# Performance work log

Hardware: AMD Instinct MI355X
Metric: run time of the kernel (lower is better)

## Reference

```python
import jax, jax.numpy as jnp
import numpy as np

T, B, D, H = 2048, 2, 1024, 16
NH, DH = H // 2, D // H   # 8 heads per direction, d_head = 64
DFF = 4096


def layer_norm(x, g, b, eps=1e-5):
    mu = jnp.mean(x, axis=-1, keepdims=True)
    var = jnp.mean(jnp.square(x - mu), axis=-1, keepdims=True)
    return (x - mu) * jax.lax.rsqrt(var + eps) * g + b


def rel_shift(x):
    # x: [q, k, b, n] -> Transformer-XL relative shift
    q, k, b, n = x.shape
    x = jnp.concatenate([jnp.zeros((q, 1, b, n), x.dtype), x], axis=1)
    return x.reshape(k + 1, q, b, n)[1:].reshape(q, k, b, n)


def rel_attn(w, r, mask, qkv_w, r_w, r_w_bias, r_r_bias):
    # w: [T, B, D], r: [R, 1, D], mask: [T, T] bool (True = masked)
    t, b, _ = w.shape
    heads = jnp.einsum('tbd,ed->tbe', w, qkv_w)              # [T,B,3*NH*DH]
    q, k, v = jnp.split(heads, 3, axis=-1)
    q = q.reshape(t, b, NH, DH)
    k = k.reshape(t, b, NH, DH)
    v = v.reshape(t, b, NH, DH)
    rk = jnp.einsum('rd,ed->re', r[:, 0, :], r_w).reshape(-1, NH, DH)  # [R,NH,DH]
    AC = jnp.einsum('ibnd,jbnd->ijbn', q + r_w_bias, k)
    BD = rel_shift(jnp.einsum('ibnd,jnd->ijbn', q + r_r_bias, rk))
    score = (AC + BD) * (1.0 / np.sqrt(DH))
    score = jnp.where(mask[:, :, None, None], jnp.finfo(score.dtype).min, score)
    prob = jax.nn.softmax(score, axis=1)
    vec = jnp.einsum('ijbn,jbnd->ibnd', prob, v)
    return vec.reshape(t, b, NH * DH)


def setup_inputs() -> dict:
    key = jax.random.key(0)
    ks = jax.random.split(key, 24)
    s = 0.02
    causal = jnp.triu(jnp.ones((T, T), dtype=bool), k=1)
    return {
        'x': jax.random.normal(ks[0], (T, B, D), jnp.float32),
        'pos': jax.random.normal(ks[1], (T, 1, D), jnp.float32),
        'mask_fwd': causal,
        'mask_bwd': causal,
        'ln1_g': jnp.ones((D,), jnp.float32), 'ln1_b': jnp.zeros((D,), jnp.float32),
        'ln2_g': jnp.ones((D,), jnp.float32), 'ln2_b': jnp.zeros((D,), jnp.float32),
        'ln3_g': jnp.ones((D,), jnp.float32), 'ln3_b': jnp.zeros((D,), jnp.float32),
        'qkv_f': jax.random.normal(ks[2], (3 * NH * DH, D), jnp.float32) * s,
        'rnet_f': jax.random.normal(ks[3], (NH * DH, D), jnp.float32) * s,
        'rwb_f': jax.random.normal(ks[4], (NH, DH), jnp.float32) * s,
        'rrb_f': jax.random.normal(ks[5], (NH, DH), jnp.float32) * s,
        'qkv_b': jax.random.normal(ks[6], (3 * NH * DH, D), jnp.float32) * s,
        'rnet_b': jax.random.normal(ks[7], (NH * DH, D), jnp.float32) * s,
        'rwb_b': jax.random.normal(ks[8], (NH, DH), jnp.float32) * s,
        'rrb_b': jax.random.normal(ks[9], (NH, DH), jnp.float32) * s,
        'wo': jax.random.normal(ks[10], (D, D), jnp.float32) * s,
        'bo': jnp.zeros((D,), jnp.float32),
        'w1': jax.random.normal(ks[11], (DFF, D), jnp.float32) * s,
        'b1': jnp.zeros((DFF,), jnp.float32),
        'w2': jax.random.normal(ks[12], (D, DFF), jnp.float32) * s,
        'b2': jnp.zeros((D,), jnp.float32),
    }


def reference(x, pos, mask_fwd, mask_bwd,
              ln1_g, ln1_b, ln2_g, ln2_b, ln3_g, ln3_b,
              qkv_f, rnet_f, rwb_f, rrb_f,
              qkv_b, rnet_b, rwb_b, rrb_b,
              wo, bo, w1, b1, w2, b2):
    # --- bidirectional relative attention ---
    q_fwd = layer_norm(x, ln1_g, ln1_b)
    q_bwd = layer_norm(jnp.flip(x, axis=0), ln2_g, ln2_b)
    out_fwd = rel_attn(q_fwd, pos, mask_fwd, qkv_f, rnet_f, rwb_f, rrb_f)
    out_bwd = rel_attn(q_bwd, pos, mask_bwd, qkv_b, rnet_b, rwb_b, rrb_b)
    out = jnp.concatenate([out_fwd, jnp.flip(out_bwd, axis=0)], axis=-1)
    out = jnp.einsum('tbd,ed->tbe', out, wo) + bo
    h = x + out                     # postprocess_attn: dropout(id) + residual
    # --- feed forward: LN -> Linear -> ReLU -> Linear -> residual ---
    y = layer_norm(h, ln3_g, ln3_b)
    y = jax.nn.relu(jnp.einsum('tbd,fd->tbf', y, w1) + b1)
    y = jnp.einsum('tbf,df->tbd', y, w2) + b2
    return h + y
```

## Files before the change

kernel.cpp:

```cpp
#include <hip/hip_runtime.h>
#include <cstdint>
#include <cstddef>


typedef unsigned short ushort_t;
typedef __bf16 bf16x8 __attribute__((ext_vector_type(8)));
typedef float f32x4 __attribute__((ext_vector_type(4)));
typedef float f32x16 __attribute__((ext_vector_type(16)));
typedef unsigned short us8 __attribute__((ext_vector_type(8)));
typedef unsigned short us4 __attribute__((ext_vector_type(4)));

#define DEV static __device__ __forceinline__

DEV ushort_t f2bf(float x) {
  union { float f; unsigned u; } v; v.f = x;
  unsigned r = (v.u + 0x7FFFu + ((v.u >> 16) & 1u)) >> 16;
  return (ushort_t)r;
}
DEV ushort_t f2bt(float x) {
  union { float f; unsigned u; } v; v.f = x;
  return (ushort_t)(v.u >> 16);
}
DEV float bf2f(ushort_t h) {
  union { unsigned u; float f; } v; v.u = ((unsigned)h) << 16;
  return v.f;
}
DEV float fexp2(float x) { float r; asm("v_exp_f32 %0, %1" : "=v"(r) : "v"(x)); return r; }
DEV f32x4 mfma16(bf16x8 a, bf16x8 b, f32x4 c) {
  return __builtin_amdgcn_mfma_f32_16x16x32_bf16(a, b, c, 0, 0, 0);
}
DEV f32x16 mfma32(bf16x8 a, bf16x8 b, f32x16 c) {
  return __builtin_amdgcn_mfma_f32_32x32x16_bf16(a, b, c, 0, 0, 0);
}
DEV void gld16(const void* g, void* l) {
  __builtin_amdgcn_global_load_lds((const __attribute__((address_space(1))) void*)g,
                                   (__attribute__((address_space(3))) void*)l,
                                   16, 0, 0);
}

constexpr size_t O_QKV_F  = 0;
constexpr size_t O_QKV_B  = 3145728;
constexpr size_t O_RNET_F = 6291456;
constexpr size_t O_RNET_B = 7340032;
constexpr size_t O_WO     = 8388608;
constexpr size_t O_W1     = 10485760;
constexpr size_t O_W2     = 18874368;
constexpr size_t O_RKREV_F= 27262976;
constexpr size_t O_RKREV_B= 29360128;
constexpr size_t O_QAC_F  = 31457280;
constexpr size_t O_QBD_F  = 35651584;
constexpr size_t O_KK_F   = 39845888;
constexpr size_t O_VT_F   = 44040192;
constexpr size_t O_QAC_B  = 48234496;
constexpr size_t O_QBD_B  = 52428800;
constexpr size_t O_KK_B   = 56623104;
constexpr size_t O_VT_B   = 60817408;
constexpr size_t O_H      = 65011712;
constexpr size_t O_LN3    = 81788928;
constexpr size_t ZONE     = 90177536;
constexpr size_t O_POS    = ZONE + 0;
constexpr size_t O_LN1    = ZONE + 4194304;
constexpr size_t O_LN2    = ZONE + 12582912;
constexpr size_t O_HEADS_F= ZONE + 20971520;
constexpr size_t O_HEADS_B= ZONE + 33554432;
constexpr size_t O_ACAT   = ZONE + 0;
constexpr size_t O_FFNM   = ZONE + 8388608;

struct CvtArgs {
  const float* src[8];
  ushort_t* dst[8];
  int bstart[8];
};
__global__ __launch_bounds__(256)
void cvt_all_k(CvtArgs a) {
  int bx = blockIdx.x;
  int s = 0;
#pragma unroll
  for (int k = 1; k < 8; ++k) if (bx >= a.bstart[k]) s = k;
  int i = (bx - a.bstart[s]) * 256 + threadIdx.x;
  float4 v = reinterpret_cast<const float4*>(a.src[s])[i];
  us4 o; o[0] = f2bf(v.x); o[1] = f2bf(v.y); o[2] = f2bf(v.z); o[3] = f2bf(v.w);
  reinterpret_cast<us4*>(a.dst[s])[i] = o;
}

__global__ __launch_bounds__(256)
void ln_dual_k(const float* __restrict__ x,
               const float* __restrict__ g1, const float* __restrict__ b1,
               const float* __restrict__ g2, const float* __restrict__ b2,
               ushort_t* __restrict__ o1, ushort_t* __restrict__ o2) {
  __shared__ float sbuf[8];
  const int row = blockIdx.x;
  const int tid = threadIdx.x;
  const float* xr = x + (size_t)row * 1024;
  float4 v = reinterpret_cast<const float4*>(xr)[tid];
  float s  = v.x + v.y + v.z + v.w;
  float s2 = v.x*v.x + v.y*v.y + v.z*v.z + v.w*v.w;
  for (int m = 32; m >= 1; m >>= 1) { s += __shfl_xor(s, m, 64); s2 += __shfl_xor(s2, m, 64); }
  int w = tid >> 6;
  if ((tid & 63) == 0) { sbuf[w] = s; sbuf[4 + w] = s2; }
  __syncthreads();
  float S  = sbuf[0] + sbuf[1] + sbuf[2] + sbuf[3];
  float S2 = sbuf[4] + sbuf[5] + sbuf[6] + sbuf[7];
  float mu  = S * (1.f / 1024.f);
  float var = S2 * (1.f / 1024.f) - mu * mu;
  float inv = rsqrtf(var + 1e-5f);
  int t = row >> 1, b = row & 1;
  size_t r2 = ((size_t)(2047 - t) * 2 + b) * 1024;
  float4 G1 = reinterpret_cast<const float4*>(g1)[tid];
  float4 B1 = reinterpret_cast<const float4*>(b1)[tid];
  float4 G2 = reinterpret_cast<const float4*>(g2)[tid];
  float4 B2 = reinterpret_cast<const float4*>(b2)[tid];
  float n0 = (v.x - mu) * inv, n1 = (v.y - mu) * inv, n2 = (v.z - mu) * inv, n3 = (v.w - mu) * inv;
  us4 a, c;
  a[0] = f2bf(n0 * G1.x + B1.x); a[1] = f2bf(n1 * G1.y + B1.y);
  a[2] = f2bf(n2 * G1.z + B1.z); a[3] = f2bf(n3 * G1.w + B1.w);
  c[0] = f2bf(n0 * G2.x + B2.x); c[1] = f2bf(n1 * G2.y + B2.y);
  c[2] = f2bf(n2 * G2.z + B2.z); c[3] = f2bf(n3 * G2.w + B2.w);
  reinterpret_cast<us4*>(o1 + (size_t)row * 1024)[tid] = a;
  reinterpret_cast<us4*>(o2 + r2)[tid] = c;
}

__global__ __launch_bounds__(256)
void ln_one_k(const float* __restrict__ x,
              const float* __restrict__ g1, const float* __restrict__ b1,
              ushort_t* __restrict__ o1) {
  __shared__ float sbuf[8];
  const int row = blockIdx.x;
  const int tid = threadIdx.x;
  const float* xr = x + (size_t)row * 1024;
  float4 v = reinterpret_cast<const float4*>(xr)[tid];
  float s  = v.x + v.y + v.z + v.w;
  float s2 = v.x*v.x + v.y*v.y + v.z*v.z + v.w*v.w;
  for (int m = 32; m >= 1; m >>= 1) { s += __shfl_xor(s, m, 64); s2 += __shfl_xor(s2, m, 64); }
  int w = tid >> 6;
  if ((tid & 63) == 0) { sbuf[w] = s; sbuf[4 + w] = s2; }
  __syncthreads();
  float S  = sbuf[0] + sbuf[1] + sbuf[2] + sbuf[3];
  float S2 = sbuf[4] + sbuf[5] + sbuf[6] + sbuf[7];
  float mu  = S * (1.f / 1024.f);
  float var = S2 * (1.f / 1024.f) - mu * mu;
  float inv = rsqrtf(var + 1e-5f);
  float4 G1 = reinterpret_cast<const float4*>(g1)[tid];
  float4 B1 = reinterpret_cast<const float4*>(b1)[tid];
  us4 a;
  a[0] = f2bf((v.x - mu) * inv * G1.x + B1.x);
  a[1] = f2bf((v.y - mu) * inv * G1.y + B1.y);
  a[2] = f2bf((v.z - mu) * inv * G1.z + B1.z);
  a[3] = f2bf((v.w - mu) * inv * G1.w + B1.w);
  reinterpret_cast<us4*>(o1 + (size_t)row * 1024)[tid] = a;
}

template <int EPI>
__global__ __launch_bounds__(256)
void gemm_bt(const ushort_t* __restrict__ A, const ushort_t* __restrict__ B,
             void* __restrict__ C, const float* __restrict__ bias,
             const float* __restrict__ resid, int M, int N, int K) {
  __shared__ ushort_t As[128 * 64];
  __shared__ ushort_t Bs[128 * 64];
  const int tid = threadIdx.x;
  const int lane = tid & 63;
  const int w = tid >> 6;
  const int wm = w >> 1, wn = w & 1;
  const int row0 = blockIdx.y * 128, col0 = blockIdx.x * 128;
  const int lr = lane & 15;
  const int lkb = (lane >> 4) * 8;
  const int rr = lane >> 3;
  const int scb = ((lane & 7) ^ rr) * 8;
  const f32x4 fz = {0.f, 0.f, 0.f, 0.f};
  f32x4 acc[4][4];
#pragma unroll
  for (int i = 0; i < 4; ++i)
#pragma unroll
    for (int j = 0; j < 4; ++j) acc[i][j] = fz;

  for (int k0 = 0; k0 < K; k0 += 64) {
    __syncthreads();
#pragma unroll
    for (int it = 0; it < 4; ++it) {
      int rbase = it * 32 + w * 8;
      gld16(A + (size_t)(row0 + rbase + rr) * K + k0 + scb, (char*)As + rbase * 128);
      gld16(B + (size_t)(col0 + rbase + rr) * K + k0 + scb, (char*)Bs + rbase * 128);
    }
    __syncthreads();
#pragma unroll
    for (int kk = 0; kk < 64; kk += 32) {
      bf16x8 af[4], bfr[4];
#pragma unroll
      for (int mi = 0; mi < 4; ++mi) {
        int r = wm * 64 + mi * 16 + lr;
        int off = (r * 128 + (kk + lkb) * 2) ^ ((r & 7) << 4);
        af[mi] = *reinterpret_cast<const bf16x8*>((char*)As + off);
      }
#pragma unroll
      for (int ni = 0; ni < 4; ++ni) {
        int r = wn * 64 + ni * 16 + lr;
        int off = (r * 128 + (kk + lkb) * 2) ^ ((r & 7) << 4);
        bfr[ni] = *reinterpret_cast<const bf16x8*>((char*)Bs + off);
      }
#pragma unroll
      for (int mi = 0; mi < 4; ++mi)
#pragma unroll
        for (int ni = 0; ni < 4; ++ni)
          acc[mi][ni] = mfma16(af[mi], bfr[ni], acc[mi][ni]);
    }
  }
#pragma unroll
  for (int mi = 0; mi < 4; ++mi)
#pragma unroll
    for (int ni = 0; ni < 4; ++ni)
#pragma unroll
      for (int r = 0; r < 4; ++r) {
        int row = row0 + wm * 64 + mi * 16 + (lane >> 4) * 4 + r;
        int col = col0 + wn * 64 + ni * 16 + lr;
        float v = acc[mi][ni][r];
        if (EPI == 0) {
          ((ushort_t*)C)[(size_t)row * N + col] = f2bf(v);
        } else if (EPI == 1) {
          v += bias[col]; v = v > 0.f ? v : 0.f;
          ((ushort_t*)C)[(size_t)row * N + col] = f2bf(v);
        } else {
          v += bias[col] + resid[(size_t)row * N + col];
          ((float*)C)[(size_t)row * N + col] = v;
        }
      }
}

template <int EPI>
__global__ __launch_bounds__(256)
void gemm64(const ushort_t* __restrict__ A0, const ushort_t* __restrict__ A1,
            const ushort_t* __restrict__ B0, const ushort_t* __restrict__ B1,
            void* __restrict__ C0, void* __restrict__ C1,
            const float* __restrict__ bias, const float* __restrict__ resid,
            int M, int N, int K) {
  __shared__ ushort_t As[64 * 64];
  __shared__ ushort_t Bs[128 * 64];
  const ushort_t* A = blockIdx.z ? A1 : A0;
  const ushort_t* B = blockIdx.z ? B1 : B0;
  void* C = blockIdx.z ? (void*)C1 : (void*)C0;
  const int tid = threadIdx.x;
  const int lane = tid & 63;
  const int w = tid >> 6;
  const int wm = w >> 1, wn = w & 1;
  const int row0 = blockIdx.y * 64, col0 = blockIdx.x * 128;
  const int lr = lane & 15;
  const int lkb = (lane >> 4) * 8;
  const int rr = lane >> 3;
  const int scb = ((lane & 7) ^ rr) * 8;
  const f32x4 fz = {0.f, 0.f, 0.f, 0.f};
  f32x4 acc[2][4];
#pragma unroll
  for (int i = 0; i < 2; ++i)
#pragma unroll
    for (int j = 0; j < 4; ++j) acc[i][j] = fz;

  for (int k0 = 0; k0 < K; k0 += 64) {
    __syncthreads();
#pragma unroll
    for (int it = 0; it < 2; ++it) {
      int rbase = it * 32 + w * 8;
      gld16(A + (size_t)(row0 + rbase + rr) * K + k0 + scb, (char*)As + rbase * 128);
    }
#pragma unroll
    for (int it = 0; it < 4; ++it) {
      int rbase = it * 32 + w * 8;
      gld16(B + (size_t)(col0 + rbase + rr) * K + k0 + scb, (char*)Bs + rbase * 128);
    }
    __syncthreads();
#pragma unroll
    for (int kk = 0; kk < 64; kk += 32) {
      bf16x8 af[2], bfr[4];
#pragma unroll
      for (int mi = 0; mi < 2; ++mi) {
        int r = wm * 32 + mi * 16 + lr;
        int off = (r * 128 + (kk + lkb) * 2) ^ ((r & 7) << 4);
        af[mi] = *reinterpret_cast<const bf16x8*>((char*)As + off);
      }
#pragma unroll
      for (int ni = 0; ni < 4; ++ni) {
        int r = wn * 64 + ni * 16 + lr;
        int off = (r * 128 + (kk + lkb) * 2) ^ ((r & 7) << 4);
        bfr[ni] = *reinterpret_cast<const bf16x8*>((char*)Bs + off);
      }
#pragma unroll
      for (int mi = 0; mi < 2; ++mi)
#pragma unroll
        for (int ni = 0; ni < 4; ++ni)
          acc[mi][ni] = mfma16(af[mi], bfr[ni], acc[mi][ni]);
    }
  }
#pragma unroll
  for (int mi = 0; mi < 2; ++mi)
#pragma unroll
    for (int ni = 0; ni < 4; ++ni)
#pragma unroll
      for (int r = 0; r < 4; ++r) {
        int row = row0 + wm * 32 + mi * 16 + (lane >> 4) * 4 + r;
        int col = col0 + wn * 64 + ni * 16 + lr;
        float v = acc[mi][ni][r];
        if (EPI == 0) {
          ((ushort_t*)C)[(size_t)row * N + col] = f2bf(v);
        } else if (EPI == 1) {
          v += bias[col]; v = v > 0.f ? v : 0.f;
          ((ushort_t*)C)[(size_t)row * N + col] = f2bf(v);
        } else if (EPI == 2) {
          v += bias[col] + resid[(size_t)row * N + col];
          ((float*)C)[(size_t)row * N + col] = v;
        } else {
          int nn = col >> 6, dh = col & 63;
          ((ushort_t*)C)[((size_t)nn * 2048 + (2047 - row)) * 64 + dh] = f2bf(v);
        }
      }
}

__global__ __launch_bounds__(256)
void qkv_post2_k(const ushort_t* __restrict__ hf, const ushort_t* __restrict__ hb2,
                 const float* __restrict__ rwf, const float* __restrict__ rrf,
                 const float* __restrict__ rwb2, const float* __restrict__ rrb2,
                 char* __restrict__ wsb) {
  const float SCL = 0.125f * 1.44269504088896f;
  const int dir = blockIdx.y;
  const ushort_t* heads = dir ? hb2 : hf;
  const float* rwb = dir ? rwb2 : rwf;
  const float* rrb = dir ? rrb2 : rrf;
  ushort_t* q_ac = (ushort_t*)(wsb + (dir ? O_QAC_B : O_QAC_F));
  ushort_t* q_bd = (ushort_t*)(wsb + (dir ? O_QBD_B : O_QBD_F));
  ushort_t* kout = (ushort_t*)(wsb + (dir ? O_KK_B : O_KK_F));
  int row = blockIdx.x;
  int t = row >> 1, b = row & 1;
#pragma unroll
  for (int c0 = 0; c0 < 1024; c0 += 256) {
    int c = c0 + threadIdx.x;
    ushort_t hv = heads[(size_t)row * 1536 + c];
    if (c < 512) {
      int n = c >> 6, dh = c & 63;
      size_t o = ((size_t)(b * 8 + n) * 2048 + t) * 64 + dh;
      float q = bf2f(hv);
      q_ac[o] = f2bf((q + rwb[c]) * SCL);
      q_bd[o] = f2bf((q + rrb[c]) * SCL);
    } else {
      int cc = c - 512;
      int n = cc >> 6, dh = cc & 63;
      kout[((size_t)(b * 8 + n) * 2048 + t) * 64 + dh] = hv;
    }
  }
}

__global__ __launch_bounds__(256)
void v_trans2_k(const ushort_t* __restrict__ hf, const ushort_t* __restrict__ hb2,
                char* __restrict__ wsb) {
  __shared__ float tile[64][65];
  const int dir = blockIdx.z;
  const ushort_t* heads = dir ? hb2 : hf;
  ushort_t* vt = (ushort_t*)(wsb + (dir ? O_VT_B : O_VT_F));
  int tt0 = blockIdx.x * 64;
  int bn = blockIdx.y;
  int b = bn >> 3, n = bn & 7;
  int tid = threadIdx.x;
#pragma unroll
  for (int i = 0; i < 16; ++i) {
    int rr = i * 4 + (tid >> 6);
    int cc = tid & 63;
    tile[rr][cc] = bf2f(heads[(size_t)((tt0 + rr) * 2 + b) * 1536 + 1024 + n * 64 + cc]);
  }
  __syncthreads();
#pragma unroll
  for (int i = 0; i < 16; ++i) {
    int dh = i * 4 + (tid >> 6);
    int tt = tid & 63;
    vt[((size_t)bn * 64 + dh) * 2048 + tt0 + tt] = f2bf(tile[tt][dh]);
  }
}

__global__ __launch_bounds__(256, 2)
void attn_k(const char* __restrict__ wsb, ushort_t* __restrict__ outp) {
  __shared__ ushort_t Kbuf[2][64 * 64];
  __shared__ ushort_t Vbuf[2][64 * 64];
  __shared__ ushort_t Gs[4][32 * 100];

  const int tid = threadIdx.x;
  const int lane = tid & 63;
  const int w = tid >> 6;
  const int il = lane & 31;
  const int hi = lane >> 5;
  const int rr = lane >> 3;
  const int scb = ((lane & 7) ^ rr) * 8;

  const int id = (int)(blockIdx.x + (blockIdx.y << 4) + (blockIdx.z << 8));
  const int xcd = id & 7;
  const int ord = id >> 3;
  const int pair = xcd * 4 + (ord & 3);
  const int it = 15 - (ord >> 2);
  const int bn = pair & 15;
  const int dir = pair >> 4;

  const ushort_t* qac  = (const ushort_t*)(wsb + (dir ? O_QAC_B : O_QAC_F));
  const ushort_t* qbd  = (const ushort_t*)(wsb + (dir ? O_QBD_B : O_QBD_F));
  const ushort_t* kkv  = (const ushort_t*)(wsb + (dir ? O_KK_B  : O_KK_F));
  const ushort_t* vtp  = (const ushort_t*)(wsb + (dir ? O_VT_B  : O_VT_F));
  const ushort_t* rkrev= (const ushort_t*)(wsb + (dir ? O_RKREV_B : O_RKREV_F));
  const int colbase = dir ? 512 : 0;

  const size_t hb = (size_t)bn * 2048;
  const size_t vbase = (size_t)bn * 64;
  const size_t nb = (size_t)(bn & 7) * 2048;
  const int b = bn >> 3;
  const int n = bn & 7;

  ushort_t* gw = Gs[w];

  const int i0 = it * 128;
  const int NT = 2 * it + 2;
  const int iw0 = i0 + w * 32;

  auto STAGE = [&](int bi, int j0) {
    ushort_t* kb = Kbuf[bi] + w * 512;
    ushort_t* vbp = Vbuf[bi] + w * 512;
    gld16(kkv + (hb + j0 + w * 8 + rr) * 64 + scb, kb);
    gld16(kkv + (hb + j0 + 32 + w * 8 + rr) * 64 + scb, kb + 2048);
    gld16(vtp + (vbase + w * 8 + rr) * 2048 + j0 + scb, vbp);
    gld16(vtp + (vbase + 32 + w * 8 + rr) * 2048 + j0 + scb, vbp + 2048);
  };

  bf16x8 qa[4], qb[4];
#pragma unroll
  for (int kf = 0; kf < 4; ++kf) {
    size_t off = (hb + iw0 + il) * 64 + kf * 16 + hi * 8;
    qa[kf] = *reinterpret_cast<const bf16x8*>(qac + off);
    qb[kf] = *reinterpret_cast<const bf16x8*>(qbd + off);
  }

  f32x16 Oa[2];
#pragma unroll
  for (int dhf = 0; dhf < 2; ++dhf)
#pragma unroll
    for (int e = 0; e < 16; ++e) Oa[dhf][e] = 0.f;
  float lsum = 0.f;

  STAGE(0, 0);
  __syncthreads();
  int cur = 0;
  for (int jt = 0; jt < NT; ++jt) {
    const int j0 = jt * 64;
    const bool active = (j0 <= iw0 + 31);

    if (active) {
      bf16x8 bd[3][4];
      const int dbase = iw0 - j0 - 63;
#pragma unroll
      for (int cf = 0; cf < 3; ++cf) {
        int d = dbase + cf * 32 + il;
        d = d < 0 ? 0 : (d > 2047 ? 2047 : d);
        const ushort_t* bp = rkrev + (nb + d) * 64 + hi * 8;
#pragma unroll
        for (int kf = 0; kf < 4; ++kf)
          bd[cf][kf] = *reinterpret_cast<const bf16x8*>(bp + kf * 16);
      }
      if (jt + 1 < NT) STAGE(cur ^ 1, j0 + 64);

      const ushort_t* Ks = Kbuf[cur];
      const ushort_t* Vs = Vbuf[cur];

      f32x16 S[2];
#pragma unroll
      for (int jlf = 0; jlf < 2; ++jlf) {
#pragma unroll
        for (int e = 0; e < 16; ++e) S[jlf][e] = 0.f;
        __builtin_amdgcn_s_setprio(1);
#pragma unroll
        for (int kf = 0; kf < 4; ++kf) {
          int r = jlf * 32 + il;
          int off = (r * 128 + (kf * 16 + hi * 8) * 2) ^ ((r & 7) << 4);
          S[jlf] = mfma32(*reinterpret_cast<const bf16x8*>((char*)Ks + off), qa[kf], S[jlf]);
        }
        __builtin_amdgcn_s_setprio(0);
      }
#pragma unroll
      for (int cf = 0; cf < 3; ++cf) {
        f32x16 G;
#pragma unroll
        for (int e = 0; e < 16; ++e) G[e] = 0.f;
        __builtin_amdgcn_s_setprio(1);
#pragma unroll
        for (int kf = 0; kf < 4; ++kf) G = mfma32(bd[cf][kf], qb[kf], G);
        __builtin_amdgcn_s_setprio(0);
#pragma unroll
        for (int q = 0; q < 4; ++q) {
          us4 pk;
          pk[0] = f2bt(G[4 * q + 0]); pk[1] = f2bt(G[4 * q + 1]);
          pk[2] = f2bt(G[4 * q + 2]); pk[3] = f2bt(G[4 * q + 3]);
          *reinterpret_cast<us4*>(gw + il * 100 + cf * 32 + 8 * q + 4 * hi) = pk;
        }
      }
      asm volatile("s_waitcnt lgkmcnt(0)" ::: "memory");
      const bool fullt = (j0 + 63 <= iw0);
      unsigned pq[2][4][2];
#pragma unroll
      for (int jlf = 0; jlf < 2; ++jlf)
#pragma unroll
        for (int q = 0; q < 4; ++q) {
          int c3 = il + 60 - jlf * 32 - 8 * q - 4 * hi;
          int base4 = c3 & ~3;
          int o = c3 & 3;
          const ushort_t* gp = gw + il * 100 + base4;
          uint64_t av = *reinterpret_cast<const uint64_t*>(gp);
          uint64_t bv = *reinterpret_cast<const uint64_t*>(gp + 4);
          uint64_t v = o ? ((av >> (16 * o)) | (bv << (64 - 16 * o))) : av;
          us4 pk;
#pragma unroll
          for (int r = 0; r < 4; ++r) {
            int jl = jlf * 32 + 8 * q + 4 * hi + r;
            float sv = S[jlf][4 * q + r] + bf2f((ushort_t)(v >> (16 * (3 - r))));
            if (!fullt) sv = (j0 + jl <= iw0 + il) ? sv : -1e30f;
            float p = fexp2(sv);
            lsum += p;
            pk[r] = f2bt(p);
          }
          pq[jlf][q][0] = (unsigned)pk[0] | ((unsigned)pk[1] << 16);
          pq[jlf][q][1] = (unsigned)pk[2] | ((unsigned)pk[3] << 16);
        }
#pragma unroll
      for (int kf = 0; kf < 4; ++kf) {
        const int jq = kf >> 1, q0 = (kf & 1) * 2, q1 = q0 + 1;
        unsigned own0 = hi ? pq[jq][q1][0] : pq[jq][q0][0];
        unsigned own1 = hi ? pq[jq][q1][1] : pq[jq][q0][1];
        unsigned sd0  = hi ? pq[jq][q0][0] : pq[jq][q1][0];
        unsigned sd1  = hi ? pq[jq][q0][1] : pq[jq][q1][1];
        unsigned rc0 = (unsigned)__shfl_xor((int)sd0, 32, 64);
        unsigned rc1 = (unsigned)__shfl_xor((int)sd1, 32, 64);
        union { unsigned u[4]; bf16x8 v; } pb;
        pb.u[0] = hi ? rc0 : own0;
        pb.u[1] = hi ? rc1 : own1;
        pb.u[2] = hi ? own0 : rc0;
        pb.u[3] = hi ? own1 : rc1;
        __builtin_amdgcn_s_setprio(1);
#pragma unroll
        for (int dhf = 0; dhf < 2; ++dhf) {
          int r = dhf * 32 + il;
          int voff = (r * 128 + (kf * 16 + hi * 8) * 2) ^ ((r & 7) << 4);
          Oa[dhf] = mfma32(*reinterpret_cast<const bf16x8*>((char*)Vs + voff), pb.v, Oa[dhf]);
        }
        __builtin_amdgcn_s_setprio(0);
      }
    } else {
      if (jt + 1 < NT) STAGE(cur ^ 1, j0 + 64);
    }
    __syncthreads();
    cur ^= 1;
  }
  lsum += __shfl_xor(lsum, 32, 64);
  float invl = 1.f / lsum;
  int ig = iw0 + il;
  int tout = dir ? (2047 - ig) : ig;
  size_t orow = ((size_t)tout * 2 + b) * 1024 + colbase + n * 64;
#pragma unroll
  for (int dhf = 0; dhf < 2; ++dhf)
#pragma unroll
    for (int q = 0; q < 4; ++q) {
      us4 pk;
#pragma unroll
      for (int r = 0; r < 4; ++r) pk[r] = f2bf(Oa[dhf][4 * q + r] * invl);
      *reinterpret_cast<us4*>(outp + orow + dhf * 32 + 8 * q + 4 * hi) = pk;
    }
}

extern "C" void kernel_launch(void* const* d_in, const int* in_sizes, int n_in,
                              void* d_out, int out_size, void* d_ws, size_t ws_size,
                              hipStream_t stream) {
  (void)in_sizes; (void)n_in; (void)out_size; (void)ws_size;
  const float* x    = (const float*)d_in[0];
  const float* pos  = (const float*)d_in[1];
  const float* ln1g = (const float*)d_in[4];
  const float* ln1b = (const float*)d_in[5];
  const float* ln2g = (const float*)d_in[6];
  const float* ln2b = (const float*)d_in[7];
  const float* ln3g = (const float*)d_in[8];
  const float* ln3b = (const float*)d_in[9];
  const float* qkvf = (const float*)d_in[10];
  const float* rnetf= (const float*)d_in[11];
  const float* rwbf = (const float*)d_in[12];
  const float* rrbf = (const float*)d_in[13];
  const float* qkvb = (const float*)d_in[14];
  const float* rnetb= (const float*)d_in[15];
  const float* rwbb = (const float*)d_in[16];
  const float* rrbb = (const float*)d_in[17];
  const float* wo   = (const float*)d_in[18];
  const float* bo   = (const float*)d_in[19];
  const float* w1   = (const float*)d_in[20];
  const float* b1   = (const float*)d_in[21];
  const float* w2   = (const float*)d_in[22];
  const float* b2   = (const float*)d_in[23];
  float* out = (float*)d_out;
  char* ws = (char*)d_ws;
  auto U = [&](size_t off) { return (ushort_t*)(ws + off); };

  CvtArgs ca;
  const float* srcs[8] = {qkvf, qkvb, rnetf, rnetb, wo, w1, w2, pos};
  size_t dsts[8] = {O_QKV_F, O_QKV_B, O_RNET_F, O_RNET_B, O_WO, O_W1, O_W2, O_POS};
  int bl[8] = {1536, 1536, 512, 512, 1024, 4096, 4096, 2048};
  int cum = 0;
  for (int s = 0; s < 8; ++s) {
    ca.src[s] = srcs[s];
    ca.dst[s] = U(dsts[s]);
    ca.bstart[s] = cum;
    cum += bl[s];
  }
  cvt_all_k<<<dim3(cum), dim3(256), 0, stream>>>(ca);

  ln_dual_k<<<dim3(4096), dim3(256), 0, stream>>>(x, ln1g, ln1b, ln2g, ln2b, U(O_LN1), U(O_LN2));

  gemm64<0><<<dim3(12, 64, 2), dim3(256), 0, stream>>>(
      U(O_LN1), U(O_LN2), U(O_QKV_F), U(O_QKV_B), U(O_HEADS_F), U(O_HEADS_B),
      nullptr, nullptr, 4096, 1536, 1024);
  gemm64<3><<<dim3(4, 32, 2), dim3(256), 0, stream>>>(
      U(O_POS), U(O_POS), U(O_RNET_F), U(O_RNET_B), U(O_RKREV_F), U(O_RKREV_B),
      nullptr, nullptr, 2048, 512, 1024);

  qkv_post2_k<<<dim3(4096, 2), dim3(256), 0, stream>>>(
      U(O_HEADS_F), U(O_HEADS_B), rwbf, rrbf, rwbb, rrbb, ws);
  v_trans2_k<<<dim3(32, 16, 2), dim3(256), 0, stream>>>(U(O_HEADS_F), U(O_HEADS_B), ws);

  attn_k<<<dim3(16, 16, 2), dim3(256), 0, stream>>>(ws, U(O_ACAT));

  gemm64<2><<<dim3(8, 64, 1), dim3(256), 0, stream>>>(
      U(O_ACAT), U(O_ACAT), U(O_WO), U(O_WO), ws + O_H, ws + O_H,
      bo, x, 4096, 1024, 1024);

  ln_one_k<<<dim3(4096), dim3(256), 0, stream>>>((const float*)(ws + O_H), ln3g, ln3b, U(O_LN3));
  gemm_bt<1><<<dim3(32, 32), dim3(256), 0, stream>>>(U(O_LN3), U(O_W1), U(O_FFNM), b1, nullptr, 4096, 4096, 1024);
  gemm64<2><<<dim3(8, 64, 1), dim3(256), 0, stream>>>(
      U(O_FFNM), U(O_FFNM), U(O_W2), U(O_W2), out, out,
      b2, (const float*)(ws + O_H), 4096, 1024, 4096);
}
```

Before: 355.8 us.

## Drop LDS staging of K/V in attention, read fragments directly from global

The attention kernel no longer double-buffers K and V tiles into shared memory through async copies with barriers. Each wave now loads its K and V MFMA fragments straight from global memory. The block shrinks to 128 threads covering 64 query rows, and the grid doubles to 32x16x2, so work per block is finer and no per-tile __syncthreads is needed. The trade-off is that the two waves in a block no longer share K/V data, so global/L2 traffic rises, and load latency is no longer hidden by explicit prefetch.

```diff
diff --git a/kernel.cpp b/kernel.cpp
--- a/kernel.cpp
+++ b/kernel.cpp
@@ -371,25 +371,21 @@
   }
 }
 
-__global__ __launch_bounds__(256, 2)
+__global__ __launch_bounds__(128)
 void attn_k(const char* __restrict__ wsb, ushort_t* __restrict__ outp) {
-  __shared__ ushort_t Kbuf[2][64 * 64];
-  __shared__ ushort_t Vbuf[2][64 * 64];
-  __shared__ ushort_t Gs[4][32 * 100];
+  __shared__ ushort_t Gs[2][3200];
 
   const int tid = threadIdx.x;
   const int lane = tid & 63;
   const int w = tid >> 6;
   const int il = lane & 31;
   const int hi = lane >> 5;
-  const int rr = lane >> 3;
-  const int scb = ((lane & 7) ^ rr) * 8;
-
-  const int id = (int)(blockIdx.x + (blockIdx.y << 4) + (blockIdx.z << 8));
+
+  const int id = (int)(blockIdx.x + (blockIdx.y << 5) + (blockIdx.z << 9));
   const int xcd = id & 7;
   const int ord = id >> 3;
   const int pair = xcd * 4 + (ord & 3);
-  const int it = 15 - (ord >> 2);
+  const int it = 31 - (ord >> 2);
   const int bn = pair & 15;
   const int dir = pair >> 4;
 
@@ -408,18 +404,9 @@
 
   ushort_t* gw = Gs[w];
 
-  const int i0 = it * 128;
-  const int NT = 2 * it + 2;
+  const int i0 = it * 64;
+  const int NT = it + 1;
   const int iw0 = i0 + w * 32;
-
-  auto STAGE = [&](int bi, int j0) {
-    ushort_t* kb = Kbuf[bi] + w * 512;
-    ushort_t* vbp = Vbuf[bi] + w * 512;
-    gld16(kkv + (hb + j0 + w * 8 + rr) * 64 + scb, kb);
-    gld16(kkv + (hb + j0 + 32 + w * 8 + rr) * 64 + scb, kb + 2048);
-    gld16(vtp + (vbase + w * 8 + rr) * 2048 + j0 + scb, vbp);
-    gld16(vtp + (vbase + 32 + w * 8 + rr) * 2048 + j0 + scb, vbp + 2048);
-  };
 
   bf16x8 qa[4], qb[4];
 #pragma unroll
@@ -436,116 +423,104 @@
     for (int e = 0; e < 16; ++e) Oa[dhf][e] = 0.f;
   float lsum = 0.f;
 
-  STAGE(0, 0);
-  __syncthreads();
-  int cur = 0;
   for (int jt = 0; jt < NT; ++jt) {
     const int j0 = jt * 64;
-    const bool active = (j0 <= iw0 + 31);
-
-    if (active) {
-      bf16x8 bd[3][4];
-      const int dbase = iw0 - j0 - 63;
-#pragma unroll
-      for (int cf = 0; cf < 3; ++cf) {
-        int d = dbase + cf * 32 + il;
-        d = d < 0 ? 0 : (d > 2047 ? 2047 : d);
-        const ushort_t* bp = rkrev + (nb + d) * 64 + hi * 8;
-#pragma unroll
-        for (int kf = 0; kf < 4; ++kf)
-          bd[cf][kf] = *reinterpret_cast<const bf16x8*>(bp + kf * 16);
-      }
-      if (jt + 1 < NT) STAGE(cur ^ 1, j0 + 64);
-
-      const ushort_t* Ks = Kbuf[cur];
-      const ushort_t* Vs = Vbuf[cur];
-
-      f32x16 S[2];
-#pragma unroll
-      for (int jlf = 0; jlf < 2; ++jlf) {
-#pragma unroll
-        for (int e = 0; e < 16; ++e) S[jlf][e] = 0.f;
-        __builtin_amdgcn_s_setprio(1);
-#pragma unroll
-        for (int kf = 0; kf < 4; ++kf) {
-          int r = jlf * 32 + il;
-          int off = (r * 128 + (kf * 16 + hi * 8) * 2) ^ ((r & 7) << 4);
-          S[jlf] = mfma32(*reinterpret_cast<const bf16x8*>((char*)Ks + off), qa[kf], S[jlf]);
+
+    f32x16 S[2];
+#pragma unroll
+    for (int jlf = 0; jlf < 2; ++jlf) {
+      bf16x8 kfr[4];
+#pragma unroll
+      for (int kf = 0; kf < 4; ++kf)
+        kfr[kf] = *reinterpret_cast<const bf16x8*>(
+            kkv + (hb + j0 + jlf * 32 + il) * 64 + kf * 16 + hi * 8);
+#pragma unroll
+      for (int e = 0; e < 16; ++e) S[jlf][e] = 0.f;
+      __builtin_amdgcn_s_setprio(1);
+#pragma unroll
+      for (int kf = 0; kf < 4; ++kf) S[jlf] = mfma32(kfr[kf], qa[kf], S[jlf]);
+      __builtin_amdgcn_s_setprio(0);
+    }
+    const int dbase = iw0 - j0 - 63;
+#pragma unroll
+    for (int cf = 0; cf < 3; ++cf) {
+      int d = dbase + cf * 32 + il;
+      d = d < 0 ? 0 : (d > 2047 ? 2047 : d);
+      const ushort_t* bp = rkrev + (nb + d) * 64 + hi * 8;
+      bf16x8 bd[4];
+#pragma unroll
+      for (int kf = 0; kf < 4; ++kf)
+        bd[kf] = *reinterpret_cast<const bf16x8*>(bp + kf * 16);
+      f32x16 G;
+#pragma unroll
+      for (int e = 0; e < 16; ++e) G[e] = 0.f;
+      __builtin_amdgcn_s_setprio(1);
+#pragma unroll
+      for (int kf = 0; kf < 4; ++kf) G = mfma32(bd[kf], qb[kf], G);
+      __builtin_amdgcn_s_setprio(0);
+#pragma unroll
+      for (int q = 0; q < 4; ++q) {
+        us4 pk;
+        pk[0] = f2bt(G[4 * q + 0]); pk[1] = f2bt(G[4 * q + 1]);
+        pk[2] = f2bt(G[4 * q + 2]); pk[3] = f2bt(G[4 * q + 3]);
+        *reinterpret_cast<us4*>(gw + il * 100 + cf * 32 + 8 * q + 4 * hi) = pk;
+      }
+    }
+    bf16x8 vfr[2][4];
+#pragma unroll
+    for (int dhf = 0; dhf < 2; ++dhf)
+#pragma unroll
+      for (int kf = 0; kf < 4; ++kf)
+        vfr[dhf][kf] = *reinterpret_cast<const bf16x8*>(
+            vtp + (vbase + dhf * 32 + il) * 2048 + j0 + kf * 16 + hi * 8);
+
+    asm volatile("s_waitcnt lgkmcnt(0)" ::: "memory");
+    const bool fullt = (j0 + 63 <= iw0);
+    unsigned pq[2][4][2];
+#pragma unroll
+    for (int jlf = 0; jlf < 2; ++jlf)
+#pragma unroll
+      for (int q = 0; q < 4; ++q) {
+        int c3 = il + 60 - jlf * 32 - 8 * q - 4 * hi;
+        int base4 = c3 & ~3;
+        int o = c3 & 3;
+        const ushort_t* gp = gw + il * 100 + base4;
+        uint64_t av = *reinterpret_cast<const uint64_t*>(gp);
+        uint64_t bv = *reinterpret_cast<const uint64_t*>(gp + 4);
+        uint64_t v = o ? ((av >> (16 * o)) | (bv << (64 - 16 * o))) : av;
+        us4 pk;
+#pragma unroll
+        for (int r = 0; r < 4; ++r) {
+          int jl = jlf * 32 + 8 * q + 4 * hi + r;
+          float sv = S[jlf][4 * q + r] + bf2f((ushort_t)(v >> (16 * (3 - r))));
+          if (!fullt) sv = (j0 + jl <= iw0 + il) ? sv : -1e30f;
+          float p = fexp2(sv);
+          lsum += p;
+          pk[r] = f2bt(p);
         }
-        __builtin_amdgcn_s_setprio(0);
-      }
-#pragma unroll
-      for (int cf = 0; cf < 3; ++cf) {
-        f32x16 G;
-#pragma unroll
-        for (int e = 0; e < 16; ++e) G[e] = 0.f;
-        __builtin_amdgcn_s_setprio(1);
-#pragma unroll
-        for (int kf = 0; kf < 4; ++kf) G = mfma32(bd[cf][kf], qb[kf], G);
-        __builtin_amdgcn_s_setprio(0);
-#pragma unroll
-        for (int q = 0; q < 4; ++q) {
-          us4 pk;
-          pk[0] = f2bt(G[4 * q + 0]); pk[1] = f2bt(G[4 * q + 1]);
-          pk[2] = f2bt(G[4 * q + 2]); pk[3] = f2bt(G[4 * q + 3]);
-          *reinterpret_cast<us4*>(gw + il * 100 + cf * 32 + 8 * q + 4 * hi) = pk;
-        }
-      }
-      asm volatile("s_waitcnt lgkmcnt(0)" ::: "memory");
-      const bool fullt = (j0 + 63 <= iw0);
-      unsigned pq[2][4][2];
-#pragma unroll
-      for (int jlf = 0; jlf < 2; ++jlf)
-#pragma unroll
-        for (int q = 0; q < 4; ++q) {
-          int c3 = il + 60 - jlf * 32 - 8 * q - 4 * hi;
-          int base4 = c3 & ~3;
-          int o = c3 & 3;
-          const ushort_t* gp = gw + il * 100 + base4;
-          uint64_t av = *reinterpret_cast<const uint64_t*>(gp);
-          uint64_t bv = *reinterpret_cast<const uint64_t*>(gp + 4);
-          uint64_t v = o ? ((av >> (16 * o)) | (bv << (64 - 16 * o))) : av;
-          us4 pk;
-#pragma unroll
-          for (int r = 0; r < 4; ++r) {
-            int jl = jlf * 32 + 8 * q + 4 * hi + r;
-            float sv = S[jlf][4 * q + r] + bf2f((ushort_t)(v >> (16 * (3 - r))));
-            if (!fullt) sv = (j0 + jl <= iw0 + il) ? sv : -1e30f;
-            float p = fexp2(sv);
-            lsum += p;
-            pk[r] = f2bt(p);
-          }
-          pq[jlf][q][0] = (unsigned)pk[0] | ((unsigned)pk[1] << 16);
-          pq[jlf][q][1] = (unsigned)pk[2] | ((unsigned)pk[3] << 16);
-        }
-#pragma unroll
-      for (int kf = 0; kf < 4; ++kf) {
-        const int jq = kf >> 1, q0 = (kf & 1) * 2, q1 = q0 + 1;
-        unsigned own0 = hi ? pq[jq][q1][0] : pq[jq][q0][0];
-        unsigned own1 = hi ? pq[jq][q1][1] : pq[jq][q0][1];
-        unsigned sd0  = hi ? pq[jq][q0][0] : pq[jq][q1][0];
-        unsigned sd1  = hi ? pq[jq][q0][1] : pq[jq][q1][1];
-        unsigned rc0 = (unsigned)__shfl_xor((int)sd0, 32, 64);
-        unsigned rc1 = (unsigned)__shfl_xor((int)sd1, 32, 64);
-        union { unsigned u[4]; bf16x8 v; } pb;
-        pb.u[0] = hi ? rc0 : own0;
-        pb.u[1] = hi ? rc1 : own1;
-        pb.u[2] = hi ? own0 : rc0;
-        pb.u[3] = hi ? own1 : rc1;
-        __builtin_amdgcn_s_setprio(1);
-#pragma unroll
-        for (int dhf = 0; dhf < 2; ++dhf) {
-          int r = dhf * 32 + il;
-          int voff = (r * 128 + (kf * 16 + hi * 8) * 2) ^ ((r & 7) << 4);
-          Oa[dhf] = mfma32(*reinterpret_cast<const bf16x8*>((char*)Vs + voff), pb.v, Oa[dhf]);
-        }
-        __builtin_amdgcn_s_setprio(0);
-      }
-    } else {
-      if (jt + 1 < NT) STAGE(cur ^ 1, j0 + 64);
-    }
-    __syncthreads();
-    cur ^= 1;
+        pq[jlf][q][0] = (unsigned)pk[0] | ((unsigned)pk[1] << 16);
+        pq[jlf][q][1] = (unsigned)pk[2] | ((unsigned)pk[3] << 16);
+      }
+#pragma unroll
+    for (int kf = 0; kf < 4; ++kf) {
+      const int jq = kf >> 1, q0 = (kf & 1) * 2, q1 = q0 + 1;
+      unsigned own0 = hi ? pq[jq][q1][0] : pq[jq][q0][0];
+      unsigned own1 = hi ? pq[jq][q1][1] : pq[jq][q0][1];
+      unsigned sd0  = hi ? pq[jq][q0][0] : pq[jq][q1][0];
+      unsigned sd1  = hi ? pq[jq][q0][1] : pq[jq][q1][1];
+      unsigned rc0 = (unsigned)__shfl_xor((int)sd0, 32, 64);
+      unsigned rc1 = (unsigned)__shfl_xor((int)sd1, 32, 64);
+      union { unsigned u[4]; bf16x8 v; } pb;
+      pb.u[0] = hi ? rc0 : own0;
+      pb.u[1] = hi ? rc1 : own1;
+      pb.u[2] = hi ? own0 : rc0;
+      pb.u[3] = hi ? own1 : rc1;
+      __builtin_amdgcn_s_setprio(1);
+#pragma unroll
+      for (int dhf = 0; dhf < 2; ++dhf)
+        Oa[dhf] = mfma32(vfr[dhf][kf], pb.v, Oa[dhf]);
+      __builtin_amdgcn_s_setprio(0);
+    }
   }
   lsum += __shfl_xor(lsum, 32, 64);
   float invl = 1.f / lsum;
@@ -619,7 +594,7 @@
       U(O_HEADS_F), U(O_HEADS_B), rwbf, rrbf, rwbb, rrbb, ws);
   v_trans2_k<<<dim3(32, 16, 2), dim3(256), 0, stream>>>(U(O_HEADS_F), U(O_HEADS_B), ws);
 
-  attn_k<<<dim3(16, 16, 2), dim3(256), 0, stream>>>(ws, U(O_ACAT));
+  attn_k<<<dim3(32, 16, 2), dim3(128), 0, stream>>>(ws, U(O_ACAT));
 
   gemm64<2><<<dim3(8, 64, 1), dim3(256), 0, stream>>>(
       U(O_ACAT), U(O_ACAT), U(O_WO), U(O_WO), ws + O_H, ws + O_H,
```

After: 381.6 us. +7.2%, slower.
